# Optimization experiments

Hardware: AMD Instinct MI355X
Metric: run time of the kernel (lower is better)

## Reference

```python
import jax, jax.numpy as jnp
import numpy as np

NUM_HEADS = 16

def _apply_rope(x, cos, sin):
    # x: (B, H, T, D); cos/sin: (T, D//2)
    B, H, T, D = x.shape
    xr = x.reshape(B, H, T, D // 2, 2)
    x0, x1 = xr[..., 0], xr[..., 1]
    c = cos[None, None, :, :]
    s = sin[None, None, :, :]
    out = jnp.stack([x0 * c - x1 * s, x0 * s + x1 * c], axis=-1)
    return out.reshape(B, H, T, D)


def setup_inputs() -> dict:
    key = jax.random.key(0)
    k1, k2, k3 = jax.random.split(key, 3)
    B, T, C = 2, 2048, 1024
    D = C // NUM_HEADS
    x = jax.random.normal(k1, (B, T, C), dtype=jnp.float32)
    qkv_w = jax.random.normal(k2, (3 * C, C), dtype=jnp.float32) * (C ** -0.5)
    proj_w = jax.random.normal(k3, (C, C), dtype=jnp.float32) * (C ** -0.5)
    # standard RoPE frequency table (theta = 10000)
    inv_freq = 1.0 / (10000.0 ** (jnp.arange(0, D, 2, dtype=jnp.float32) / D))  # (D/2,)
    angles = jnp.arange(T, dtype=jnp.float32)[:, None] * inv_freq[None, :]      # (T, D/2)
    return {
        "x": x,
        "freqs_cos": jnp.cos(angles),
        "freqs_sin": jnp.sin(angles),
        "qkv_w": qkv_w,
        "proj_w": proj_w,
    }


def reference(x, freqs_cos, freqs_sin, qkv_w, proj_w):
    B, T, C = x.shape
    H = NUM_HEADS
    D = C // H
    qkv = x @ qkv_w.T                                  # (B, T, 3C)
    q, k, v = jnp.split(qkv, 3, axis=-1)
    q = q.reshape(B, T, H, D).transpose(0, 2, 1, 3)    # (B, H, T, D)
    k = k.reshape(B, T, H, D).transpose(0, 2, 1, 3)
    v = v.reshape(B, T, H, D).transpose(0, 2, 1, 3)
    q = _apply_rope(q, freqs_cos, freqs_sin)
    k = _apply_rope(k, freqs_cos, freqs_sin)
    scale = 1.0 / jnp.sqrt(jnp.asarray(D, dtype=x.dtype))
    scores = jnp.einsum('bhqd,bhkd->bhqk', q, k) * scale
    causal = jnp.tril(jnp.ones((T, T), dtype=bool))
    scores = jnp.where(causal[None, None], scores, jnp.finfo(scores.dtype).min)
    attn = jax.nn.softmax(scores, axis=-1)
    out = jnp.einsum('bhqk,bhkd->bhqd', attn, v)       # (B, H, T, D)
    out = out.transpose(0, 2, 1, 3).reshape(B, T, C)
    return out @ proj_w.T
```

## Files before the change

kernel.cpp:

```cpp
#include <hip/hip_runtime.h>
#include <stdint.h>

#define DI __device__ __forceinline__

typedef unsigned short u16;
typedef __bf16 bf16x8 __attribute__((ext_vector_type(8)));
typedef unsigned short u16x8 __attribute__((ext_vector_type(8)));
typedef unsigned short u16x4 __attribute__((ext_vector_type(4)));
typedef float f32x4 __attribute__((ext_vector_type(4)));
typedef float f32x16 __attribute__((ext_vector_type(16)));
typedef unsigned int u32x2 __attribute__((ext_vector_type(2)));
typedef unsigned int u32x4 __attribute__((ext_vector_type(4)));

DI u16 f2bf(float f) { __bf16 h = (__bf16)f; return __builtin_bit_cast(u16, h); }
DI float bf2f(u16 u) { return (float)__builtin_bit_cast(__bf16, u); }

DI bf16x8 ld8(const u16* p) { return __builtin_bit_cast(bf16x8, *(const u16x8*)p); }

DI f32x4 mfma16(bf16x8 a, bf16x8 b, f32x4 c) {
  return __builtin_amdgcn_mfma_f32_16x16x32_bf16(a, b, c, 0, 0, 0);
}
DI f32x16 mfma32(bf16x8 a, bf16x8 b, f32x16 c) {
  return __builtin_amdgcn_mfma_f32_32x32x16_bf16(a, b, c, 0, 0, 0);
}

DI unsigned pkbf(float a, float b) {
  unsigned r;
  asm("v_cvt_pk_bf16_f32 %0, %1, %2" : "=v"(r) : "v"(a), "v"(b));
  return r;
}

DI void async16(const u16* g, u16* l) {
  __builtin_amdgcn_global_load_lds((const __attribute__((address_space(1))) void*)g,
                                   (__attribute__((address_space(3))) void*)l, 16, 0, 0);
}

DI void barC() {
  asm volatile("" ::: "memory");
  __builtin_amdgcn_s_barrier();
  asm volatile("" ::: "memory");
}

__global__ __launch_bounds__(256) void cast_all(const float* __restrict__ x,
                                                const float* __restrict__ qw,
                                                const float* __restrict__ pw,
                                                u16* __restrict__ xb, u16* __restrict__ qwb,
                                                u16* __restrict__ pwb) {
  const int bi = blockIdx.x;
  const float* src;
  u16* dst;
  int off;
  if (bi < 4096) {
    src = x; dst = xb; off = bi;
  } else if (bi < 7168) {
    src = qw; dst = qwb; off = bi - 4096;
  } else {
    src = pw; dst = pwb; off = bi - 7168;
  }
  const int i = off * 256 + threadIdx.x;
  const float4 v = ((const float4*)src)[i];
  u16x4 o = {f2bf(v.x), f2bf(v.y), f2bf(v.z), f2bf(v.w)};
  ((u16x4*)dst)[i] = o;
}

__global__ __launch_bounds__(512, 2) void gemm256(const u16* __restrict__ A,
                                                  const u16* __restrict__ W,
                                                  u16* __restrict__ outp,
                                                  int M, int N, int K) {
  __shared__ u16 sAB[65536];
  const int tid = threadIdx.x;
  const int w = tid >> 6, L = tid & 63;
  const int lo = L & 15, quad = L >> 4;
  const int wm128 = (w >> 2) * 128, wn64 = (w & 3) * 64;
  const int nbn = N >> 8;
  const int nwg = gridDim.x;
  const int cpx = nwg >> 3;
  const int raw = blockIdx.x;
  const int bi = (raw & 7) * cpx + (raw >> 3);
  const int bm = bi / nbn, bn = bi - bm * nbn;
  const int m0 = bm << 8, n0 = bn << 8;
  const int kSteps = K >> 6;

  f32x4 acc[8][4];
#pragma unroll
  for (int i = 0; i < 8; ++i)
#pragma unroll
    for (int j = 0; j < 4; ++j) acc[i][j] = 0.f;

  const int rS = tid >> 2;
  const int scol = ((tid & 3) << 3) ^ ((tid & 32) ? 16 : 0);
  const u16* Ap = A + (size_t)(m0 + rS) * K + scol;
  const u16* Wp = W + (size_t)(n0 + rS) * K + scol;
  auto STAGE = [&](int s, int mat, int kk) {
    if (s >= kSteps) return;
    const u16* g = (mat ? Wp : Ap) + s * 64 + kk * 32;
    u16* l = sAB + ((s & 1) << 15) + (mat << 14) + (kk << 13) + tid * 8;
    async16(g, l);
    async16(g + (size_t)128 * K, l + 4096);
  };

  const int qoff = (quad << 3) ^ ((lo & 8) ? 16 : 0);
  auto ldA = [&](int buf, int kk, int mh, int m2) {
    const int R = wm128 + mh * 64 + m2 * 16 + lo;
    return ld8(&sAB[(buf << 15) + (kk << 13) + R * 32 + qoff]);
  };
  auto ldB = [&](int buf, int kk, int nf) {
    const int R = wn64 + nf * 16 + lo;
    return ld8(&sAB[(buf << 15) + 16384 + (kk << 13) + R * 32 + qoff]);
  };

  bf16x8 bF[4];
  auto PH = [&](int buf, int kk, int mh, bool loadB, int sS, int sM, int sK,
                bool dovm, bool last) {
    bf16x8 aF[4];
#pragma unroll
    for (int m2 = 0; m2 < 4; ++m2) aF[m2] = ldA(buf, kk, mh, m2);
    if (loadB) {
#pragma unroll
      for (int nf = 0; nf < 4; ++nf) bF[nf] = ldB(buf, kk, nf);
    }
    STAGE(sS, sM, sK);
    if (dovm) {
      if (last)
        asm volatile("s_waitcnt vmcnt(0)" ::: "memory");
      else
        asm volatile("s_waitcnt vmcnt(4)" ::: "memory");
    }
    barC();
    __builtin_amdgcn_s_setprio(1);
#pragma unroll
    for (int m2 = 0; m2 < 4; ++m2)
#pragma unroll
      for (int nf = 0; nf < 4; ++nf)
        acc[mh * 4 + m2][nf] = mfma16(aF[m2], bF[nf], acc[mh * 4 + m2][nf]);
    __builtin_amdgcn_s_setprio(0);
    barC();
  };

  STAGE(0, 0, 0); STAGE(0, 1, 0); STAGE(0, 0, 1); STAGE(0, 1, 1);
  STAGE(1, 0, 0); STAGE(1, 1, 0);
  asm volatile("s_waitcnt vmcnt(4)" ::: "memory");
  barC();

  for (int t = 0; t < kSteps; t += 2) {
    const bool last = (t + 2) >= kSteps;
    PH(0, 0, 0, true,  t + 1, 0, 1, false, last);
    PH(0, 0, 1, false, t + 1, 1, 1, false, last);
    PH(0, 1, 0, true,  t + 2, 0, 0, false, last);
    PH(0, 1, 1, false, t + 2, 1, 0, true,  last);
    PH(1, 0, 0, true,  t + 2, 0, 1, false, last);
    PH(1, 0, 1, false, t + 2, 1, 1, false, last);
    PH(1, 1, 0, true,  t + 3, 0, 0, false, last);
    PH(1, 1, 1, false, t + 3, 1, 0, true,  last);
  }

#pragma unroll
  for (int mf = 0; mf < 8; ++mf) {
    const int m = m0 + wm128 + (mf >> 2) * 64 + (mf & 3) * 16 + quad * 4;
#pragma unroll
    for (int nf = 0; nf < 4; ++nf) {
      const int nn = n0 + wn64 + nf * 16 + lo;
#pragma unroll
      for (int r = 0; r < 4; ++r) outp[(size_t)(m + r) * N + nn] = f2bf(acc[mf][nf][r]);
    }
  }
}

template <int OUT_BF16>
__global__ __launch_bounds__(256) void gemm_bt(const u16* __restrict__ A,
                                               const u16* __restrict__ W,
                                               void* __restrict__ outp,
                                               int M, int N, int K) {
  __shared__ u16 sA[2 * 4096];
  __shared__ u16 sB[2 * 4096];
  const int tid = threadIdx.x;
  const int w = tid >> 6, L = tid & 63;
  const int lo = L & 15, quad = L >> 4;
  const int nb = N >> 7;
  const int bm = blockIdx.x / nb, bn = blockIdx.x - bm * nb;
  const int m0 = bm << 7, n0 = bn << 7;
  const int wm = (w >> 1) << 6, wn = (w & 1) << 6;

  f32x4 acc[4][4];
#pragma unroll
  for (int i = 0; i < 4; ++i)
#pragma unroll
    for (int j = 0; j < 4; ++j) acc[i][j] = 0.f;

  const int r0 = tid >> 2, s0 = tid & 3;
  const int c0 = s0 ^ ((r0 >> 1) & 3);
  const int r1 = r0 + 64;
  const int c1 = s0 ^ ((r1 >> 1) & 3);
  const u16* aP0 = A + (size_t)(m0 + r0) * K + c0 * 8;
  const u16* aP1 = A + (size_t)(m0 + r1) * K + c1 * 8;
  const u16* bP0 = W + (size_t)(n0 + r0) * K + c0 * 8;
  const u16* bP1 = W + (size_t)(n0 + r1) * K + c1 * 8;
  u16* ldA0 = &sA[tid * 8];
  u16* ldA1 = &sA[(tid + 256) * 8];
  u16* ldB0 = &sB[tid * 8];
  u16* ldB1 = &sB[(tid + 256) * 8];

  int raf[4], rbf[4];
#pragma unroll
  for (int mt = 0; mt < 4; ++mt) {
    int r = wm + mt * 16 + lo;
    raf[mt] = r * 32 + ((quad ^ ((r >> 1) & 3)) << 3);
    r = wn + mt * 16 + lo;
    rbf[mt] = r * 32 + ((quad ^ ((r >> 1) & 3)) << 3);
  }

  auto stage = [&](int buf) {
    const int bo = buf << 12;
    async16(aP0, ldA0 + bo);
    async16(aP1, ldA1 + bo);
    async16(bP0, ldB0 + bo);
    async16(bP1, ldB1 + bo);
    aP0 += 32; aP1 += 32; bP0 += 32; bP1 += 32;
  };

  const int kIters = K >> 5;
  stage(0);
  for (int kt = 0; kt < kIters; ++kt) {
    __syncthreads();
    if (kt + 1 < kIters) stage((kt + 1) & 1);
    const int bo = (kt & 1) << 12;
    bf16x8 af[4], bfr[4];
#pragma unroll
    for (int mt = 0; mt < 4; ++mt) af[mt] = ld8(&sA[bo + raf[mt]]);
#pragma unroll
    for (int nt = 0; nt < 4; ++nt) bfr[nt] = ld8(&sB[bo + rbf[nt]]);
#pragma unroll
    for (int mt = 0; mt < 4; ++mt)
#pragma unroll
      for (int nt = 0; nt < 4; ++nt)
        acc[mt][nt] = mfma16(af[mt], bfr[nt], acc[mt][nt]);
  }

#pragma unroll
  for (int mt = 0; mt < 4; ++mt) {
    const int m = m0 + wm + mt * 16 + quad * 4;
#pragma unroll
    for (int nt = 0; nt < 4; ++nt) {
      const int n = n0 + wn + nt * 16 + lo;
#pragma unroll
      for (int r = 0; r < 4; ++r) {
        const size_t off = (size_t)(m + r) * N + n;
        if (OUT_BF16)
          ((u16*)outp)[off] = f2bf(acc[mt][nt][r]);
        else
          ((float*)outp)[off] = acc[mt][nt][r];
      }
    }
  }
}

#define QSCALE 0.18033688011112f
__global__ __launch_bounds__(256) void ropevt_k(const u16* __restrict__ qkv,
                                                const float* __restrict__ cosb,
                                                const float* __restrict__ sinb,
                                                u16* __restrict__ qo, u16* __restrict__ ko,
                                                u16* __restrict__ vto) {
  __shared__ u16 sT[64 * 64];
  const int tid = threadIdx.x;
  if (blockIdx.x < 2048) {
    const int idx = blockIdx.x * 256 + tid;
    const int c = idx & 7;
    const int h = (idx >> 3) & 15;
    const int t = (idx >> 7) & 2047;
    const int b = idx >> 18;
    const size_t src = (size_t)(b * 2048 + t) * 3072 + h * 64 + c * 8;
    const u16x8 qv = *(const u16x8*)&qkv[src];
    const u16x8 kv = *(const u16x8*)&qkv[src + 1024];
    const f32x4 cv = *(const f32x4*)&cosb[t * 32 + c * 4];
    const f32x4 sv = *(const f32x4*)&sinb[t * 32 + c * 4];
    u16x8 q8, k8;
#pragma unroll
    for (int j = 0; j < 4; ++j) {
      const float cc = cv[j], ss = sv[j];
      const float q0 = bf2f(qv[2 * j]), q1 = bf2f(qv[2 * j + 1]);
      q8[2 * j] = f2bf((q0 * cc - q1 * ss) * QSCALE);
      q8[2 * j + 1] = f2bf((q0 * ss + q1 * cc) * QSCALE);
      const float k0 = bf2f(kv[2 * j]), k1 = bf2f(kv[2 * j + 1]);
      k8[2 * j] = f2bf(k0 * cc - k1 * ss);
      k8[2 * j + 1] = f2bf(k0 * ss + k1 * cc);
    }
    const size_t dst = (size_t)((b * 16 + h) * 2048 + t) * 64 + c * 8;
    *(u16x8*)&qo[dst] = q8;
    *(u16x8*)&ko[dst] = k8;
  } else {
    const int bi = blockIdx.x - 2048;
    const int bh = bi & 31;
    const int t0 = (bi >> 5) << 6;
    const int b = bh >> 4, h = bh & 15;
#pragma unroll
    for (int it = 0; it < 2; ++it) {
      const int id = tid + it * 256;
      const int tr = id >> 3, s = id & 7, c = s ^ (tr & 7);
      async16(qkv + (size_t)(b * 2048 + t0 + tr) * 3072 + 2048 + h * 64 + c * 8, &sT[id * 8]);
    }
    __syncthreads();
#pragma unroll
    for (int it = 0; it < 2; ++it) {
      const int id = tid + it * 256;
      const int d = id >> 3, ct = id & 7;
      u16x8 o;
#pragma unroll
      for (int j = 0; j < 8; ++j) {
        const int t = ct * 8 + j;
        o[j] = sT[t * 64 + (((d >> 3) ^ (t & 7)) << 3) + (d & 7)];
      }
      *(u16x8*)(vto + ((size_t)bh * 64 + d) * 2048 + t0 + ct * 8) = o;
    }
  }
}

__global__ __launch_bounds__(256, 2) void fattn_part(const u16* __restrict__ qs,
                                                     const u16* __restrict__ ks,
                                                     const u16* __restrict__ vtb,
                                                     u16* __restrict__ opart,
                                                     float* __restrict__ lbuf) {
  __shared__ u16 sK[2 * 4096];
  __shared__ u16 sVt[2 * 4096];
  const int tid = threadIdx.x;
  const int w = tid >> 6, L = tid & 63;
  const int col = L & 31, hi = L >> 5;
  const int raw = blockIdx.x;
  const int part = raw & 1;
  const int bh = (raw >> 1) & 31;
  const int qb = 15 - (raw >> 6);
  const int n = 2 * qb + 2;
  const int h0 = qb + 1;
  const int tk0 = part ? h0 : 0;
  const int tk1 = part ? n : h0;
  const size_t hoff = (size_t)bh * (2048 * 64);
  const int q0 = qb << 7;
  const int wq = q0 + w * 32;

  const int kvA = tid >> 3, cA = (tid & 7) ^ (kvA & 7);
  const int idB = tid + 256;
  const int kvB = idB >> 3, cB = (idB & 7) ^ (kvB & 7);
  const u16* kP0 = ks + hoff + (size_t)(tk0 * 64 + kvA) * 64 + cA * 8;
  const u16* kP1 = ks + hoff + (size_t)(tk0 * 64 + kvB) * 64 + cB * 8;
  const u16* vP0 = vtb + hoff + (size_t)kvA * 2048 + tk0 * 64 + cA * 8;
  const u16* vP1 = vtb + hoff + (size_t)kvB * 2048 + tk0 * 64 + cB * 8;
  u16* ldK0 = &sK[tid * 8];
  u16* ldK1 = &sK[idB * 8];
  u16* ldV0 = &sVt[tid * 8];
  u16* ldV1 = &sVt[idB * 8];

  auto stage = [&](int buf) {
    const int bo = buf << 12;
    async16(kP0, ldK0 + bo);
    async16(kP1, ldK1 + bo);
    async16(vP0, ldV0 + bo);
    async16(vP1, ldV1 + bo);
    kP0 += 4096; kP1 += 4096; vP0 += 64; vP1 += 64;
  };

  int kaOff[2][4];
#pragma unroll
  for (int mt = 0; mt < 2; ++mt) {
    const int row = mt * 32 + col;
#pragma unroll
    for (int ksI = 0; ksI < 4; ++ksI)
      kaOff[mt][ksI] = row * 64 + (((ksI * 2 + hi) ^ (row & 7)) << 3);
  }

  bf16x8 qf[4];
#pragma unroll
  for (int ksI = 0; ksI < 4; ++ksI)
    qf[ksI] = ld8(qs + hoff + (size_t)(wq + col) * 64 + ksI * 16 + hi * 8);

  bf16x8 ones;
#pragma unroll
  for (int j = 0; j < 8; ++j) ones[j] = (__bf16)1.0f;

  f32x16 lacc = 0.f;
  f32x16 ot0 = 0.f, ot1 = 0.f;

  const int ntk = tk1 - tk0;
  stage(0);
  for (int it2 = 0; it2 < ntk; ++it2) {
    __syncthreads();
    if (it2 + 1 < ntk) stage((it2 + 1) & 1);
    const int bo = (it2 & 1) << 12;
    const int kt = tk0 + it2;

    if (64 * kt <= wq + 31) {
      f32x16 st0 = 0.f, st1 = 0.f;
      __builtin_amdgcn_s_setprio(1);
#pragma unroll
      for (int ksI = 0; ksI < 4; ++ksI) {
        st0 = mfma32(ld8(&sK[bo + kaOff[0][ksI]]), qf[ksI], st0);
        st1 = mfma32(ld8(&sK[bo + kaOff[1][ksI]]), qf[ksI], st1);
      }
      __builtin_amdgcn_s_setprio(0);
      if (64 * kt + 63 > wq) {
        const int qg = wq + col;
        const int kvb = 64 * kt + 4 * hi;
#pragma unroll
        for (int r = 0; r < 16; ++r) {
          const int kvr = kvb + (r & 3) + 8 * (r >> 2);
          if (kvr > qg) st0[r] = -3.0e38f;
          if (kvr + 32 > qg) st1[r] = -3.0e38f;
        }
      }
      bf16x8 pf[4];
#pragma unroll
      for (int mt = 0; mt < 2; ++mt) {
        const f32x16 sv = mt ? st1 : st0;
        f32x16 p;
#pragma unroll
        for (int r = 0; r < 16; ++r) p[r] = __builtin_amdgcn_exp2f(sv[r]);
        {
          unsigned x0 = pkbf(p[0], p[1]), x1 = pkbf(p[2], p[3]);
          unsigned y0 = pkbf(p[4], p[5]), y1 = pkbf(p[6], p[7]);
          u32x2 r02 = __builtin_amdgcn_permlane32_swap(x0, y0, false, false);
          u32x2 r13 = __builtin_amdgcn_permlane32_swap(x1, y1, false, false);
          u32x4 wv = {r02[0], r13[0], r02[1], r13[1]};
          pf[2 * mt] = __builtin_bit_cast(bf16x8, wv);
        }
        {
          unsigned x0 = pkbf(p[8], p[9]), x1 = pkbf(p[10], p[11]);
          unsigned y0 = pkbf(p[12], p[13]), y1 = pkbf(p[14], p[15]);
          u32x2 r02 = __builtin_amdgcn_permlane32_swap(x0, y0, false, false);
          u32x2 r13 = __builtin_amdgcn_permlane32_swap(x1, y1, false, false);
          u32x4 wv = {r02[0], r13[0], r02[1], r13[1]};
          pf[2 * mt + 1] = __builtin_bit_cast(bf16x8, wv);
        }
      }
      __builtin_amdgcn_s_setprio(1);
#pragma unroll
      for (int ksI = 0; ksI < 4; ++ksI) lacc = mfma32(ones, pf[ksI], lacc);
#pragma unroll
      for (int ksI = 0; ksI < 4; ++ksI) {
        ot0 = mfma32(ld8(&sVt[bo + kaOff[0][ksI]]), pf[ksI], ot0);
        ot1 = mfma32(ld8(&sVt[bo + kaOff[1][ksI]]), pf[ksI], ot1);
      }
      __builtin_amdgcn_s_setprio(0);
    }
  }

  const int q = wq + col;
  const int pq = bh * 32 + (q >> 6);
  u16* ob = opart + (size_t)(part * 1024 + pq) * 4096 + (size_t)(q & 63) * 64;
#pragma unroll
  for (int mtd = 0; mtd < 2; ++mtd) {
    const f32x16 o = mtd ? ot1 : ot0;
#pragma unroll
    for (int rg = 0; rg < 4; ++rg) {
      const int d0 = mtd * 32 + rg * 8 + hi * 4;
      u16x4 ok = {f2bf(o[rg * 4 + 0]), f2bf(o[rg * 4 + 1]),
                  f2bf(o[rg * 4 + 2]), f2bf(o[rg * 4 + 3])};
      *(u16x4*)&ob[d0] = ok;
    }
  }
  if (hi == 0) lbuf[(size_t)(part * 1024 + pq) * 64 + (q & 63)] = lacc[0];
}

__global__ __launch_bounds__(256) void fattn_merge(const u16* __restrict__ opart,
                                                   const float* __restrict__ lbuf,
                                                   u16* __restrict__ aout) {
  const int pq = blockIdx.x;
  const int bh = pq >> 5, qi = pq & 31;
  const int b = bh >> 4, h = bh & 15;
  const int tid = threadIdx.x;
#pragma unroll
  for (int it = 0; it < 2; ++it) {
    const int idx = tid + it * 256;
    const int q = idx >> 3, d0 = (idx & 7) * 8;
    const float l0 = lbuf[(size_t)pq * 64 + q];
    const float l1 = lbuf[(size_t)(1024 + pq) * 64 + q];
    const float inv = 1.f / (l0 + l1);
    const u16x8 o0 = *(const u16x8*)&opart[(size_t)pq * 4096 + q * 64 + d0];
    const u16x8 o1 = *(const u16x8*)&opart[(size_t)(1024 + pq) * 4096 + q * 64 + d0];
    u16x8 o;
#pragma unroll
    for (int j = 0; j < 8; ++j) o[j] = f2bf((bf2f(o0[j]) + bf2f(o1[j])) * inv);
    *(u16x8*)&aout[((size_t)(b * 2048 + qi * 64 + q)) * 1024 + h * 64 + d0] = o;
  }
}

extern "C" void kernel_launch(void* const* d_in, const int* in_sizes, int n_in,
                              void* d_out, int out_size, void* d_ws, size_t ws_size,
                              hipStream_t stream) {
  const float* x = (const float*)d_in[0];
  const float* fcos = (const float*)d_in[1];
  const float* fsin = (const float*)d_in[2];
  const float* qkvw = (const float*)d_in[3];
  const float* projw = (const float*)d_in[4];
  float* out = (float*)d_out;

  char* ws = (char*)d_ws;
  u16* x_bf = (u16*)(ws);
  u16* qkvw_bf = (u16*)(ws + (8u << 20));
  u16* projw_bf = (u16*)(ws + (14u << 20));
  u16* qkv_bf = (u16*)(ws + (16u << 20));
  u16* q_bf = (u16*)(ws + (40u << 20));
  u16* k_bf = (u16*)(ws + (48u << 20));
  u16* vt = (u16*)(ws + (56u << 20));
  u16* attn_bf = (u16*)(ws + (64u << 20));
  u16* opart = (u16*)(ws + (16u << 20));
  float* lbuf = (float*)(ws + (32u << 20));

  cast_all<<<8192, 256, 0, stream>>>(x, qkvw, projw, x_bf, qkvw_bf, projw_bf);
  gemm256<<<192, 512, 0, stream>>>(x_bf, qkvw_bf, qkv_bf, 4096, 3072, 1024);
  ropevt_k<<<3072, 256, 0, stream>>>(qkv_bf, fcos, fsin, q_bf, k_bf, vt);
  fattn_part<<<1024, 256, 0, stream>>>(q_bf, k_bf, vt, opart, lbuf);
  fattn_merge<<<1024, 256, 0, stream>>>(opart, lbuf, attn_bf);
  gemm_bt<0><<<256, 256, 0, stream>>>(attn_bf, projw_bf, (void*)out, 4096, 1024, 1024);
}
```

Measured before the change: 181.8 us.

## Drop split-KV attention partition and merge kernel, normalize in-kernel

Replaces the two-part split-KV flash attention (1024 blocks plus a separate merge kernel) with a single kernel of 512 blocks that processes the full causal KV range per query block and normalizes by the row sum before writing. This removes the partial-output and row-sum round trip through global memory and one kernel launch. In exchange it halves the grid, so per-block work is longer and more uneven. Blocks are ordered longest-first then ascending to help balance the load.

```diff
diff --git a/kernel.cpp b/kernel.cpp
--- a/kernel.cpp
+++ b/kernel.cpp
@@ -314,24 +314,19 @@
   }
 }
 
-__global__ __launch_bounds__(256, 2) void fattn_part(const u16* __restrict__ qs,
-                                                     const u16* __restrict__ ks,
-                                                     const u16* __restrict__ vtb,
-                                                     u16* __restrict__ opart,
-                                                     float* __restrict__ lbuf) {
+__global__ __launch_bounds__(256, 2) void fattn(const u16* __restrict__ qs,
+                                                const u16* __restrict__ ks,
+                                                const u16* __restrict__ vtb,
+                                                u16* __restrict__ aout) {
   __shared__ u16 sK[2 * 4096];
   __shared__ u16 sVt[2 * 4096];
   const int tid = threadIdx.x;
   const int w = tid >> 6, L = tid & 63;
   const int col = L & 31, hi = L >> 5;
   const int raw = blockIdx.x;
-  const int part = raw & 1;
-  const int bh = (raw >> 1) & 31;
-  const int qb = 15 - (raw >> 6);
-  const int n = 2 * qb + 2;
-  const int h0 = qb + 1;
-  const int tk0 = part ? h0 : 0;
-  const int tk1 = part ? n : h0;
+  const int bh = raw & 31;
+  const int qb = (raw < 256) ? (15 - (raw >> 5)) : ((raw - 256) >> 5);
+  const int ntk = 2 * qb + 2;
   const size_t hoff = (size_t)bh * (2048 * 64);
   const int q0 = qb << 7;
   const int wq = q0 + w * 32;
@@ -339,10 +334,10 @@
   const int kvA = tid >> 3, cA = (tid & 7) ^ (kvA & 7);
   const int idB = tid + 256;
   const int kvB = idB >> 3, cB = (idB & 7) ^ (kvB & 7);
-  const u16* kP0 = ks + hoff + (size_t)(tk0 * 64 + kvA) * 64 + cA * 8;
-  const u16* kP1 = ks + hoff + (size_t)(tk0 * 64 + kvB) * 64 + cB * 8;
-  const u16* vP0 = vtb + hoff + (size_t)kvA * 2048 + tk0 * 64 + cA * 8;
-  const u16* vP1 = vtb + hoff + (size_t)kvB * 2048 + tk0 * 64 + cB * 8;
+  const u16* kP0 = ks + hoff + (size_t)kvA * 64 + cA * 8;
+  const u16* kP1 = ks + hoff + (size_t)kvB * 64 + cB * 8;
+  const u16* vP0 = vtb + hoff + (size_t)kvA * 2048 + cA * 8;
+  const u16* vP1 = vtb + hoff + (size_t)kvB * 2048 + cB * 8;
   u16* ldK0 = &sK[tid * 8];
   u16* ldK1 = &sK[idB * 8];
   u16* ldV0 = &sVt[tid * 8];
@@ -378,13 +373,11 @@
   f32x16 lacc = 0.f;
   f32x16 ot0 = 0.f, ot1 = 0.f;
 
-  const int ntk = tk1 - tk0;
   stage(0);
-  for (int it2 = 0; it2 < ntk; ++it2) {
+  for (int kt = 0; kt < ntk; ++kt) {
     __syncthreads();
-    if (it2 + 1 < ntk) stage((it2 + 1) & 1);
-    const int bo = (it2 & 1) << 12;
-    const int kt = tk0 + it2;
+    if (kt + 1 < ntk) stage((kt + 1) & 1);
+    const int bo = (kt & 1) << 12;
 
     if (64 * kt <= wq + 31) {
       f32x16 st0 = 0.f, st1 = 0.f;
@@ -441,43 +434,20 @@
     }
   }
 
-  const int q = wq + col;
-  const int pq = bh * 32 + (q >> 6);
-  u16* ob = opart + (size_t)(part * 1024 + pq) * 4096 + (size_t)(q & 63) * 64;
+  const int t = wq + col;
+  const int b = bh >> 4, h = bh & 15;
+  const float inv = 1.f / lacc[0];
+  u16* ob = aout + ((size_t)(b * 2048 + t)) * 1024 + h * 64;
 #pragma unroll
   for (int mtd = 0; mtd < 2; ++mtd) {
     const f32x16 o = mtd ? ot1 : ot0;
 #pragma unroll
     for (int rg = 0; rg < 4; ++rg) {
       const int d0 = mtd * 32 + rg * 8 + hi * 4;
-      u16x4 ok = {f2bf(o[rg * 4 + 0]), f2bf(o[rg * 4 + 1]),
-                  f2bf(o[rg * 4 + 2]), f2bf(o[rg * 4 + 3])};
+      u16x4 ok = {f2bf(o[rg * 4 + 0] * inv), f2bf(o[rg * 4 + 1] * inv),
+                  f2bf(o[rg * 4 + 2] * inv), f2bf(o[rg * 4 + 3] * inv)};
       *(u16x4*)&ob[d0] = ok;
     }
-  }
-  if (hi == 0) lbuf[(size_t)(part * 1024 + pq) * 64 + (q & 63)] = lacc[0];
-}
-
-__global__ __launch_bounds__(256) void fattn_merge(const u16* __restrict__ opart,
-                                                   const float* __restrict__ lbuf,
-                                                   u16* __restrict__ aout) {
-  const int pq = blockIdx.x;
-  const int bh = pq >> 5, qi = pq & 31;
-  const int b = bh >> 4, h = bh & 15;
-  const int tid = threadIdx.x;
-#pragma unroll
-  for (int it = 0; it < 2; ++it) {
-    const int idx = tid + it * 256;
-    const int q = idx >> 3, d0 = (idx & 7) * 8;
-    const float l0 = lbuf[(size_t)pq * 64 + q];
-    const float l1 = lbuf[(size_t)(1024 + pq) * 64 + q];
-    const float inv = 1.f / (l0 + l1);
-    const u16x8 o0 = *(const u16x8*)&opart[(size_t)pq * 4096 + q * 64 + d0];
-    const u16x8 o1 = *(const u16x8*)&opart[(size_t)(1024 + pq) * 4096 + q * 64 + d0];
-    u16x8 o;
-#pragma unroll
-    for (int j = 0; j < 8; ++j) o[j] = f2bf((bf2f(o0[j]) + bf2f(o1[j])) * inv);
-    *(u16x8*)&aout[((size_t)(b * 2048 + qi * 64 + q)) * 1024 + h * 64 + d0] = o;
   }
 }
 
@@ -500,13 +470,10 @@
   u16* k_bf = (u16*)(ws + (48u << 20));
   u16* vt = (u16*)(ws + (56u << 20));
   u16* attn_bf = (u16*)(ws + (64u << 20));
-  u16* opart = (u16*)(ws + (16u << 20));
-  float* lbuf = (float*)(ws + (32u << 20));
 
   cast_all<<<8192, 256, 0, stream>>>(x, qkvw, projw, x_bf, qkvw_bf, projw_bf);
   gemm256<<<192, 512, 0, stream>>>(x_bf, qkvw_bf, qkv_bf, 4096, 3072, 1024);
   ropevt_k<<<3072, 256, 0, stream>>>(qkv_bf, fcos, fsin, q_bf, k_bf, vt);
-  fattn_part<<<1024, 256, 0, stream>>>(q_bf, k_bf, vt, opart, lbuf);
-  fattn_merge<<<1024, 256, 0, stream>>>(opart, lbuf, attn_bf);
+  fattn<<<512, 256, 0, stream>>>(q_bf, k_bf, vt, attn_bf);
   gemm_bt<0><<<256, 256, 0, stream>>>(attn_bf, projw_bf, (void*)out, 4096, 1024, 1024);
 }
```

New measurement: 189.0 us. 1.04x slower.

## Fuse split-attention merge into output projection GEMM A-tile loading

Applied to the files above, without the earlier changes.

Removes the separate fattn_merge kernel and instead has the projection GEMM read both partial attention outputs and their softmax denominators directly, combining and normalising them while staging the A tile into shared memory. This drops one kernel launch and the write and re-read of the merged attention buffer. In exchange, A loads go through registers instead of async copies, each A element is read from two partial buffers, and the reciprocal is recomputed per tile across the 8 N-blocks, adding redundant global traffic and latency in the K loop.

```diff
diff --git a/kernel.cpp b/kernel.cpp
--- a/kernel.cpp
+++ b/kernel.cpp
@@ -162,94 +162,6 @@
       const int nn = n0 + wn64 + nf * 16 + lo;
 #pragma unroll
       for (int r = 0; r < 4; ++r) outp[(size_t)(m + r) * N + nn] = f2bf(acc[mf][nf][r]);
-    }
-  }
-}
-
-template <int OUT_BF16>
-__global__ __launch_bounds__(256) void gemm_bt(const u16* __restrict__ A,
-                                               const u16* __restrict__ W,
-                                               void* __restrict__ outp,
-                                               int M, int N, int K) {
-  __shared__ u16 sA[2 * 4096];
-  __shared__ u16 sB[2 * 4096];
-  const int tid = threadIdx.x;
-  const int w = tid >> 6, L = tid & 63;
-  const int lo = L & 15, quad = L >> 4;
-  const int nb = N >> 7;
-  const int bm = blockIdx.x / nb, bn = blockIdx.x - bm * nb;
-  const int m0 = bm << 7, n0 = bn << 7;
-  const int wm = (w >> 1) << 6, wn = (w & 1) << 6;
-
-  f32x4 acc[4][4];
-#pragma unroll
-  for (int i = 0; i < 4; ++i)
-#pragma unroll
-    for (int j = 0; j < 4; ++j) acc[i][j] = 0.f;
-
-  const int r0 = tid >> 2, s0 = tid & 3;
-  const int c0 = s0 ^ ((r0 >> 1) & 3);
-  const int r1 = r0 + 64;
-  const int c1 = s0 ^ ((r1 >> 1) & 3);
-  const u16* aP0 = A + (size_t)(m0 + r0) * K + c0 * 8;
-  const u16* aP1 = A + (size_t)(m0 + r1) * K + c1 * 8;
-  const u16* bP0 = W + (size_t)(n0 + r0) * K + c0 * 8;
-  const u16* bP1 = W + (size_t)(n0 + r1) * K + c1 * 8;
-  u16* ldA0 = &sA[tid * 8];
-  u16* ldA1 = &sA[(tid + 256) * 8];
-  u16* ldB0 = &sB[tid * 8];
-  u16* ldB1 = &sB[(tid + 256) * 8];
-
-  int raf[4], rbf[4];
-#pragma unroll
-  for (int mt = 0; mt < 4; ++mt) {
-    int r = wm + mt * 16 + lo;
-    raf[mt] = r * 32 + ((quad ^ ((r >> 1) & 3)) << 3);
-    r = wn + mt * 16 + lo;
-    rbf[mt] = r * 32 + ((quad ^ ((r >> 1) & 3)) << 3);
-  }
-
-  auto stage = [&](int buf) {
-    const int bo = buf << 12;
-    async16(aP0, ldA0 + bo);
-    async16(aP1, ldA1 + bo);
-    async16(bP0, ldB0 + bo);
-    async16(bP1, ldB1 + bo);
-    aP0 += 32; aP1 += 32; bP0 += 32; bP1 += 32;
-  };
-
-  const int kIters = K >> 5;
-  stage(0);
-  for (int kt = 0; kt < kIters; ++kt) {
-    __syncthreads();
-    if (kt + 1 < kIters) stage((kt + 1) & 1);
-    const int bo = (kt & 1) << 12;
-    bf16x8 af[4], bfr[4];
-#pragma unroll
-    for (int mt = 0; mt < 4; ++mt) af[mt] = ld8(&sA[bo + raf[mt]]);
-#pragma unroll
-    for (int nt = 0; nt < 4; ++nt) bfr[nt] = ld8(&sB[bo + rbf[nt]]);
-#pragma unroll
-    for (int mt = 0; mt < 4; ++mt)
-#pragma unroll
-      for (int nt = 0; nt < 4; ++nt)
-        acc[mt][nt] = mfma16(af[mt], bfr[nt], acc[mt][nt]);
-  }
-
-#pragma unroll
-  for (int mt = 0; mt < 4; ++mt) {
-    const int m = m0 + wm + mt * 16 + quad * 4;
-#pragma unroll
-    for (int nt = 0; nt < 4; ++nt) {
-      const int n = n0 + wn + nt * 16 + lo;
-#pragma unroll
-      for (int r = 0; r < 4; ++r) {
-        const size_t off = (size_t)(m + r) * N + n;
-        if (OUT_BF16)
-          ((u16*)outp)[off] = f2bf(acc[mt][nt][r]);
-        else
-          ((float*)outp)[off] = acc[mt][nt][r];
-      }
     }
   }
 }
@@ -458,26 +370,121 @@
   if (hi == 0) lbuf[(size_t)(part * 1024 + pq) * 64 + (q & 63)] = lacc[0];
 }
 
-__global__ __launch_bounds__(256) void fattn_merge(const u16* __restrict__ opart,
-                                                   const float* __restrict__ lbuf,
-                                                   u16* __restrict__ aout) {
-  const int pq = blockIdx.x;
-  const int bh = pq >> 5, qi = pq & 31;
-  const int b = bh >> 4, h = bh & 15;
+__global__ __launch_bounds__(256) void gemm_proj(const u16* __restrict__ opart,
+                                                 const float* __restrict__ lbuf,
+                                                 const u16* __restrict__ W,
+                                                 float* __restrict__ outp) {
+  const int N = 1024, K = 1024;
+  __shared__ u16 sA[2 * 4096];
+  __shared__ u16 sB[2 * 4096];
   const int tid = threadIdx.x;
-#pragma unroll
-  for (int it = 0; it < 2; ++it) {
-    const int idx = tid + it * 256;
-    const int q = idx >> 3, d0 = (idx & 7) * 8;
-    const float l0 = lbuf[(size_t)pq * 64 + q];
-    const float l1 = lbuf[(size_t)(1024 + pq) * 64 + q];
-    const float inv = 1.f / (l0 + l1);
-    const u16x8 o0 = *(const u16x8*)&opart[(size_t)pq * 4096 + q * 64 + d0];
-    const u16x8 o1 = *(const u16x8*)&opart[(size_t)(1024 + pq) * 4096 + q * 64 + d0];
-    u16x8 o;
-#pragma unroll
-    for (int j = 0; j < 8; ++j) o[j] = f2bf((bf2f(o0[j]) + bf2f(o1[j])) * inv);
-    *(u16x8*)&aout[((size_t)(b * 2048 + qi * 64 + q)) * 1024 + h * 64 + d0] = o;
+  const int w = tid >> 6, L = tid & 63;
+  const int lo = L & 15, quad = L >> 4;
+  const int bm = blockIdx.x >> 3, bn = blockIdx.x & 7;
+  const int m0 = bm << 7, n0 = bn << 7;
+  const int wm = (w >> 1) << 6, wn = (w & 1) << 6;
+
+  f32x4 acc[4][4];
+#pragma unroll
+  for (int i = 0; i < 4; ++i)
+#pragma unroll
+    for (int j = 0; j < 4; ++j) acc[i][j] = 0.f;
+
+  const int r0 = tid >> 2, s0 = tid & 3;
+  const int c0 = s0 ^ ((r0 >> 1) & 3);
+  const int r1 = r0 + 64;
+  const int c1 = s0 ^ ((r1 >> 1) & 3);
+
+  const int m_0 = m0 + r0, m_1 = m0 + r1;
+  const int q_0 = m_0 & 63, q_1 = m_1 & 63;
+  const int pqb0 = (m_0 >> 11) * 512 + ((m_0 & 2047) >> 6);
+  const int pqb1 = (m_1 >> 11) * 512 + ((m_1 & 2047) >> 6);
+
+  const u16* bP0 = W + (size_t)(n0 + r0) * K + c0 * 8;
+  const u16* bP1 = W + (size_t)(n0 + r1) * K + c1 * 8;
+  u16* ldB0 = &sB[tid * 8];
+  u16* ldB1 = &sB[(tid + 256) * 8];
+
+  int raf[4], rbf[4];
+#pragma unroll
+  for (int mt = 0; mt < 4; ++mt) {
+    int r = wm + mt * 16 + lo;
+    raf[mt] = r * 32 + ((quad ^ ((r >> 1) & 3)) << 3);
+    r = wn + mt * 16 + lo;
+    rbf[mt] = r * 32 + ((quad ^ ((r >> 1) & 3)) << 3);
+  }
+
+  u16x8 oa0, ob0, oa1, ob1;
+  float inv0, inv1;
+
+  auto aload = [&](int kt) {
+    const int kb0 = kt * 32 + c0 * 8;
+    const int pq0 = pqb0 + (kb0 >> 6) * 32;
+    const int d0 = kb0 & 63;
+    oa0 = *(const u16x8*)&opart[(size_t)pq0 * 4096 + q_0 * 64 + d0];
+    ob0 = *(const u16x8*)&opart[(size_t)(1024 + pq0) * 4096 + q_0 * 64 + d0];
+    inv0 = 1.f / (lbuf[(size_t)pq0 * 64 + q_0] + lbuf[(size_t)(1024 + pq0) * 64 + q_0]);
+    const int kb1 = kt * 32 + c1 * 8;
+    const int pq1 = pqb1 + (kb1 >> 6) * 32;
+    const int d1 = kb1 & 63;
+    oa1 = *(const u16x8*)&opart[(size_t)pq1 * 4096 + q_1 * 64 + d1];
+    ob1 = *(const u16x8*)&opart[(size_t)(1024 + pq1) * 4096 + q_1 * 64 + d1];
+    inv1 = 1.f / (lbuf[(size_t)pq1 * 64 + q_1] + lbuf[(size_t)(1024 + pq1) * 64 + q_1]);
+  };
+  auto bstage = [&](int buf) {
+    const int bo = buf << 12;
+    async16(bP0, ldB0 + bo);
+    async16(bP1, ldB1 + bo);
+    bP0 += 32;
+    bP1 += 32;
+  };
+  auto awrite = [&](int buf) {
+    const int bo = buf << 12;
+    u16x8 v0, v1;
+#pragma unroll
+    for (int j = 0; j < 8; ++j) {
+      v0[j] = f2bf((bf2f(oa0[j]) + bf2f(ob0[j])) * inv0);
+      v1[j] = f2bf((bf2f(oa1[j]) + bf2f(ob1[j])) * inv1);
+    }
+    *(u16x8*)&sA[bo + tid * 8] = v0;
+    *(u16x8*)&sA[bo + (tid + 256) * 8] = v1;
+  };
+
+  aload(0);
+  bstage(0);
+  awrite(0);
+
+  const int kIters = K >> 5;
+  for (int kt = 0; kt < kIters; ++kt) {
+    __syncthreads();
+    const bool more = (kt + 1 < kIters);
+    if (more) {
+      aload(kt + 1);
+      bstage((kt + 1) & 1);
+    }
+    const int bo = (kt & 1) << 12;
+    bf16x8 af[4], bfr[4];
+#pragma unroll
+    for (int mt = 0; mt < 4; ++mt) af[mt] = ld8(&sA[bo + raf[mt]]);
+#pragma unroll
+    for (int nt = 0; nt < 4; ++nt) bfr[nt] = ld8(&sB[bo + rbf[nt]]);
+#pragma unroll
+    for (int mt = 0; mt < 4; ++mt)
+#pragma unroll
+      for (int nt = 0; nt < 4; ++nt)
+        acc[mt][nt] = mfma16(af[mt], bfr[nt], acc[mt][nt]);
+    if (more) awrite((kt + 1) & 1);
+  }
+
+#pragma unroll
+  for (int mt = 0; mt < 4; ++mt) {
+    const int m = m0 + wm + mt * 16 + quad * 4;
+#pragma unroll
+    for (int nt = 0; nt < 4; ++nt) {
+      const int n = n0 + wn + nt * 16 + lo;
+#pragma unroll
+      for (int r = 0; r < 4; ++r) outp[(size_t)(m + r) * N + n] = acc[mt][nt][r];
+    }
   }
 }
 
@@ -499,7 +506,6 @@
   u16* q_bf = (u16*)(ws + (40u << 20));
   u16* k_bf = (u16*)(ws + (48u << 20));
   u16* vt = (u16*)(ws + (56u << 20));
-  u16* attn_bf = (u16*)(ws + (64u << 20));
   u16* opart = (u16*)(ws + (16u << 20));
   float* lbuf = (float*)(ws + (32u << 20));
 
@@ -507,6 +513,5 @@
   gemm256<<<192, 512, 0, stream>>>(x_bf, qkvw_bf, qkv_bf, 4096, 3072, 1024);
   ropevt_k<<<3072, 256, 0, stream>>>(qkv_bf, fcos, fsin, q_bf, k_bf, vt);
   fattn_part<<<1024, 256, 0, stream>>>(q_bf, k_bf, vt, opart, lbuf);
-  fattn_merge<<<1024, 256, 0, stream>>>(opart, lbuf, attn_bf);
-  gemm_bt<0><<<256, 256, 0, stream>>>(attn_bf, projw_bf, (void*)out, 4096, 1024, 1024);
-}
+  gemm_proj<<<256, 256, 0, stream>>>(opart, lbuf, projw_bf, out);
+}
```

New measurement: 199.0 us. 1.09x slower.

## Fuse RoPE and Q scaling into QKV GEMM epilogue, keep separate V transpose

Applied to the files above, without the earlier changes.

Moves the RoPE rotation and Q scaling into the epilogue of the QKV GEMM. Rotation partners are fetched with a lane shuffle, and Q and K are written straight to head-major layout. V is written to a compact buffer and transposed by a smaller dedicated kernel. This avoids writing and re-reading the full QKV intermediate for Q and K. In exchange, the epilogue does scalar strided stores and per-element cos/sin loads, which may coalesce poorly.

```diff
diff --git a/kernel.cpp b/kernel.cpp
--- a/kernel.cpp
+++ b/kernel.cpp
@@ -40,6 +40,8 @@
   __builtin_amdgcn_s_barrier();
   asm volatile("" ::: "memory");
 }
+
+#define QSCALE 0.18033688011112f
 
 __global__ __launch_bounds__(256) void cast_all(const float* __restrict__ x,
                                                 const float* __restrict__ qw,
@@ -63,10 +65,14 @@
   ((u16x4*)dst)[i] = o;
 }
 
-__global__ __launch_bounds__(512, 2) void gemm256(const u16* __restrict__ A,
-                                                  const u16* __restrict__ W,
-                                                  u16* __restrict__ outp,
-                                                  int M, int N, int K) {
+__global__ __launch_bounds__(512, 2) void gemm256_rope(const u16* __restrict__ A,
+                                                       const u16* __restrict__ W,
+                                                       u16* __restrict__ qo,
+                                                       u16* __restrict__ ko,
+                                                       u16* __restrict__ vbuf,
+                                                       const float* __restrict__ fcos,
+                                                       const float* __restrict__ fsin,
+                                                       int M, int N, int K) {
   __shared__ u16 sAB[65536];
   const int tid = threadIdx.x;
   const int w = tid >> 6, L = tid & 63;
@@ -156,12 +162,30 @@
 
 #pragma unroll
   for (int mf = 0; mf < 8; ++mf) {
-    const int m = m0 + wm128 + (mf >> 2) * 64 + (mf & 3) * 16 + quad * 4;
+    const int mB = m0 + wm128 + (mf >> 2) * 64 + (mf & 3) * 16 + quad * 4;
 #pragma unroll
     for (int nf = 0; nf < 4; ++nf) {
-      const int nn = n0 + wn64 + nf * 16 + lo;
-#pragma unroll
-      for (int r = 0; r < 4; ++r) outp[(size_t)(m + r) * N + nn] = f2bf(acc[mf][nf][r]);
+      const int n = n0 + wn64 + nf * 16 + lo;
+      const int d = n & 63, h = (n >> 6) & 15;
+      const int ri = d >> 1;
+      const bool oddd = d & 1;
+      const int seg = n >> 10;
+#pragma unroll
+      for (int r = 0; r < 4; ++r) {
+        const int m = mB + r;
+        const int b = m >> 11, t = m & 2047;
+        const float v = acc[mf][nf][r];
+        if (seg == 2) {
+          vbuf[(size_t)(b * 2048 + t) * 1024 + (n - 2048)] = f2bf(v);
+        } else {
+          const float pv = __shfl_xor(v, 1);
+          const float c = fcos[t * 32 + ri], s = fsin[t * 32 + ri];
+          float o = oddd ? (pv * s + v * c) : (v * c - pv * s);
+          if (seg == 0) o *= QSCALE;
+          u16* dst = seg ? ko : qo;
+          dst[((size_t)(b * 16 + h) * 2048 + t) * 64 + d] = f2bf(o);
+        }
+      }
     }
   }
 }
@@ -254,63 +278,32 @@
   }
 }
 
-#define QSCALE 0.18033688011112f
-__global__ __launch_bounds__(256) void ropevt_k(const u16* __restrict__ qkv,
-                                                const float* __restrict__ cosb,
-                                                const float* __restrict__ sinb,
-                                                u16* __restrict__ qo, u16* __restrict__ ko,
-                                                u16* __restrict__ vto) {
+__global__ __launch_bounds__(256) void vt_k(const u16* __restrict__ vbuf,
+                                            u16* __restrict__ vto) {
   __shared__ u16 sT[64 * 64];
   const int tid = threadIdx.x;
-  if (blockIdx.x < 2048) {
-    const int idx = blockIdx.x * 256 + tid;
-    const int c = idx & 7;
-    const int h = (idx >> 3) & 15;
-    const int t = (idx >> 7) & 2047;
-    const int b = idx >> 18;
-    const size_t src = (size_t)(b * 2048 + t) * 3072 + h * 64 + c * 8;
-    const u16x8 qv = *(const u16x8*)&qkv[src];
-    const u16x8 kv = *(const u16x8*)&qkv[src + 1024];
-    const f32x4 cv = *(const f32x4*)&cosb[t * 32 + c * 4];
-    const f32x4 sv = *(const f32x4*)&sinb[t * 32 + c * 4];
-    u16x8 q8, k8;
-#pragma unroll
-    for (int j = 0; j < 4; ++j) {
-      const float cc = cv[j], ss = sv[j];
-      const float q0 = bf2f(qv[2 * j]), q1 = bf2f(qv[2 * j + 1]);
-      q8[2 * j] = f2bf((q0 * cc - q1 * ss) * QSCALE);
-      q8[2 * j + 1] = f2bf((q0 * ss + q1 * cc) * QSCALE);
-      const float k0 = bf2f(kv[2 * j]), k1 = bf2f(kv[2 * j + 1]);
-      k8[2 * j] = f2bf(k0 * cc - k1 * ss);
-      k8[2 * j + 1] = f2bf(k0 * ss + k1 * cc);
-    }
-    const size_t dst = (size_t)((b * 16 + h) * 2048 + t) * 64 + c * 8;
-    *(u16x8*)&qo[dst] = q8;
-    *(u16x8*)&ko[dst] = k8;
-  } else {
-    const int bi = blockIdx.x - 2048;
-    const int bh = bi & 31;
-    const int t0 = (bi >> 5) << 6;
-    const int b = bh >> 4, h = bh & 15;
-#pragma unroll
-    for (int it = 0; it < 2; ++it) {
-      const int id = tid + it * 256;
-      const int tr = id >> 3, s = id & 7, c = s ^ (tr & 7);
-      async16(qkv + (size_t)(b * 2048 + t0 + tr) * 3072 + 2048 + h * 64 + c * 8, &sT[id * 8]);
-    }
-    __syncthreads();
-#pragma unroll
-    for (int it = 0; it < 2; ++it) {
-      const int id = tid + it * 256;
-      const int d = id >> 3, ct = id & 7;
-      u16x8 o;
-#pragma unroll
-      for (int j = 0; j < 8; ++j) {
-        const int t = ct * 8 + j;
-        o[j] = sT[t * 64 + (((d >> 3) ^ (t & 7)) << 3) + (d & 7)];
-      }
-      *(u16x8*)(vto + ((size_t)bh * 64 + d) * 2048 + t0 + ct * 8) = o;
-    }
+  const int bi = blockIdx.x;
+  const int bh = bi & 31;
+  const int t0 = (bi >> 5) << 6;
+  const int b = bh >> 4, h = bh & 15;
+#pragma unroll
+  for (int it = 0; it < 2; ++it) {
+    const int id = tid + it * 256;
+    const int tr = id >> 3, s = id & 7, c = s ^ (tr & 7);
+    async16(vbuf + (size_t)(b * 2048 + t0 + tr) * 1024 + h * 64 + c * 8, &sT[id * 8]);
+  }
+  __syncthreads();
+#pragma unroll
+  for (int it = 0; it < 2; ++it) {
+    const int id = tid + it * 256;
+    const int d = id >> 3, ct = id & 7;
+    u16x8 o;
+#pragma unroll
+    for (int j = 0; j < 8; ++j) {
+      const int t = ct * 8 + j;
+      o[j] = sT[t * 64 + (((d >> 3) ^ (t & 7)) << 3) + (d & 7)];
+    }
+    *(u16x8*)(vto + ((size_t)bh * 64 + d) * 2048 + t0 + ct * 8) = o;
   }
 }
 
@@ -495,7 +488,7 @@
   u16* x_bf = (u16*)(ws);
   u16* qkvw_bf = (u16*)(ws + (8u << 20));
   u16* projw_bf = (u16*)(ws + (14u << 20));
-  u16* qkv_bf = (u16*)(ws + (16u << 20));
+  u16* v_buf = (u16*)(ws + (16u << 20));
   u16* q_bf = (u16*)(ws + (40u << 20));
   u16* k_bf = (u16*)(ws + (48u << 20));
   u16* vt = (u16*)(ws + (56u << 20));
@@ -504,8 +497,9 @@
   float* lbuf = (float*)(ws + (32u << 20));
 
   cast_all<<<8192, 256, 0, stream>>>(x, qkvw, projw, x_bf, qkvw_bf, projw_bf);
-  gemm256<<<192, 512, 0, stream>>>(x_bf, qkvw_bf, qkv_bf, 4096, 3072, 1024);
-  ropevt_k<<<3072, 256, 0, stream>>>(qkv_bf, fcos, fsin, q_bf, k_bf, vt);
+  gemm256_rope<<<192, 512, 0, stream>>>(x_bf, qkvw_bf, q_bf, k_bf, v_buf, fcos, fsin,
+                                        4096, 3072, 1024);
+  vt_k<<<1024, 256, 0, stream>>>(v_buf, vt);
   fattn_part<<<1024, 256, 0, stream>>>(q_bf, k_bf, vt, opart, lbuf);
   fattn_merge<<<1024, 256, 0, stream>>>(opart, lbuf, attn_bf);
   gemm_bt<0><<<256, 256, 0, stream>>>(attn_bf, projw_bf, (void*)out, 4096, 1024, 1024);
```

Result: slower. 202.0 us (+11.1%).
